# Performance work log

Hardware: AMD Instinct MI355X
Metric: run time of the kernel (lower is better)

## Reference

```python
import jax, jax.numpy as jnp
import numpy as np

EMBED = 1024
HEADS = 16
HEAD_DIM = EMBED // HEADS


def setup_inputs() -> dict:
    key = jax.random.key(0)
    ks = jax.random.split(key, 8)
    B, S = 2, 2048
    inp = {
        "values": jax.random.normal(ks[0], (B, S, EMBED), jnp.float32),
        "keys": jax.random.normal(ks[1], (B, S, EMBED), jnp.float32),
        "queries": jax.random.normal(ks[2], (B, S, EMBED), jnp.float32),
        # per-head projection weights (torch Linear: y = x @ W.T), shared across heads
        "Wv": jax.random.normal(ks[3], (HEAD_DIM, HEAD_DIM), jnp.float32) / np.sqrt(HEAD_DIM),
        "Wk": jax.random.normal(ks[4], (HEAD_DIM, HEAD_DIM), jnp.float32) / np.sqrt(HEAD_DIM),
        "Wq": jax.random.normal(ks[5], (HEAD_DIM, HEAD_DIM), jnp.float32) / np.sqrt(HEAD_DIM),
        "Wo": jax.random.normal(ks[6], (EMBED, EMBED), jnp.float32) / np.sqrt(EMBED),
        "bo": jax.random.normal(ks[7], (EMBED,), jnp.float32) * 0.02,
    }
    return inp


def reference(values, keys, queries, Wv, Wk, Wq, Wo, bo):
    B, S, _ = queries.shape
    # split heads: (B, H, S, D)
    def split(x):
        return x.reshape(B, -1, HEADS, HEAD_DIM).transpose(0, 2, 1, 3)
    v, k, q = split(values), split(keys), split(queries)
    # per-head linear projections (no bias): x @ W.T
    v = jnp.einsum('bhsd,ed->bhse', v, Wv)
    k = jnp.einsum('bhsd,ed->bhse', k, Wk)
    q = jnp.einsum('bhsd,ed->bhse', q, Wq)
    # scaled dot-product attention (naive, full matrix)
    scores = jnp.einsum('bhqd,bhkd->bhqk', q, k) / jnp.sqrt(jnp.float32(HEAD_DIM))
    attn = jax.nn.softmax(scores, axis=-1)
    out = jnp.einsum('bhqk,bhkd->bhqd', attn, v)
    # merge heads and output projection
    out = out.transpose(0, 2, 1, 3).reshape(B, S, EMBED)
    return out @ Wo.T + bo
```

## Files before the change

kernel.cpp:

```cpp
#include <hip/hip_runtime.h>
#include <stdint.h>

#define HEADS 16
#define HD    64
#define SEQ   2048
#define BATCH 2
#define EMB   1024

using short8  = __attribute__((ext_vector_type(8))) short;
using float4v = __attribute__((ext_vector_type(4))) float;

__device__ __forceinline__ unsigned int f2bfr(float f) {
    return (__float_as_uint(f) + 0x8000u) >> 16;
}

__device__ __forceinline__ unsigned int dpp_xor1(unsigned int x) {
    return (unsigned int)__builtin_amdgcn_update_dpp(0, (int)x, 0xB1, 0xF, 0xF, true);
}

__global__ __launch_bounds__(256) void cvt_wo_kernel(const float* __restrict__ Wo,
                                                     unsigned short* __restrict__ Wob) {
    int i = (blockIdx.x * 256 + threadIdx.x) * 4;
    float4 v = *(const float4*)(Wo + i);
    uint2 o;
    o.x = f2bfr(v.x) | (f2bfr(v.y) << 16);
    o.y = f2bfr(v.z) | (f2bfr(v.w) << 16);
    *(uint2*)(Wob + i) = o;
}

__global__ __launch_bounds__(256) void proj_kernel(
    const float* __restrict__ Vx, const float* __restrict__ Kx, const float* __restrict__ Qx,
    const float* __restrict__ Wv, const float* __restrict__ Wk, const float* __restrict__ Wq,
    unsigned short* __restrict__ Qp, unsigned short* __restrict__ Kp,
    unsigned short* __restrict__ Vt) {
    __shared__ __align__(16) unsigned short Ws[64 * 72];
    __shared__ __align__(16) unsigned short xs[64 * 72];
    __shared__ __align__(16) unsigned short vt2[64 * 72];

    const int t = threadIdx.x, w = t >> 6, lane = t & 63, cl = lane & 15, quad = lane >> 4;
    const int z  = blockIdx.z;
    const int bh = blockIdx.y;
    const int b  = bh >> 4, h = bh & 15;
    const int s0 = blockIdx.x * 64;

    const float* x = (z == 0) ? Qx : (z == 1) ? Kx : Vx;
    const float* W = (z == 0) ? Wq : (z == 1) ? Wk : Wv;
    const float scale = (z == 0) ? 0.18033688011112044f : 1.0f;

#pragma unroll
    for (int rep = 0; rep < 4; ++rep) {
        int idx = rep * 1024 + t * 4;
        int e = idx >> 6, d0 = idx & 63;
        float4 w4 = *(const float4*)(W + idx);
        uint2 pk;
        pk.x = f2bfr(w4.x * scale) | (f2bfr(w4.y * scale) << 16);
        pk.y = f2bfr(w4.z * scale) | (f2bfr(w4.w * scale) << 16);
        *(uint2*)(&Ws[e * 72 + d0]) = pk;

        int s = e;
        float4 v4 = *(const float4*)(x + (size_t)(b * SEQ + s0 + s) * EMB + h * 64 + d0);
        uint2 px;
        px.x = f2bfr(v4.x) | (f2bfr(v4.y) << 16);
        px.y = f2bfr(v4.z) | (f2bfr(v4.w) << 16);
        *(uint2*)(&xs[s * 72 + d0]) = px;
    }
    __syncthreads();

    short8 a0 = *(const short8*)(&xs[(w * 16 + cl) * 72 + quad * 8]);
    short8 a1 = *(const short8*)(&xs[(w * 16 + cl) * 72 + 32 + quad * 8]);
    float4v c[4];
#pragma unroll
    for (int nt = 0; nt < 4; ++nt) c[nt] = (float4v){0.f, 0.f, 0.f, 0.f};
#pragma unroll
    for (int nt = 0; nt < 4; ++nt) {
        short8 b0 = *(const short8*)(&Ws[(nt * 16 + cl) * 72 + quad * 8]);
        c[nt] = __builtin_amdgcn_mfma_f32_16x16x32_bf16(a0, b0, c[nt], 0, 0, 0);
        short8 b1 = *(const short8*)(&Ws[(nt * 16 + cl) * 72 + 32 + quad * 8]);
        c[nt] = __builtin_amdgcn_mfma_f32_16x16x32_bf16(a1, b1, c[nt], 0, 0, 0);
    }

    if (z < 2) {
#pragma unroll
        for (int nt = 0; nt < 4; ++nt)
#pragma unroll
            for (int r = 0; r < 4; ++r)
                xs[(w * 16 + quad * 4 + r) * 72 + nt * 16 + cl] =
                    (unsigned short)f2bfr(c[nt][r]);
        unsigned short* outp = (z == 0) ? Qp : Kp;
        int sl = w * 16 + (lane >> 2), c0 = (lane & 3) * 16;
        uint4 o0 = *(const uint4*)(&xs[sl * 72 + c0]);
        uint4 o1 = *(const uint4*)(&xs[sl * 72 + c0 + 8]);
        size_t base = ((size_t)bh * SEQ + s0 + sl) * 64 + c0;
        *(uint4*)(outp + base)     = o0;
        *(uint4*)(outp + base + 8) = o1;
    } else {
#pragma unroll
        for (int nt = 0; nt < 4; ++nt)
#pragma unroll
            for (int r = 0; r < 4; ++r)
                vt2[(nt * 16 + cl) * 72 + w * 16 + quad * 4 + r] =
                    (unsigned short)f2bfr(c[nt][r]);
        __syncthreads();
        int e = t >> 2, sc0 = (t & 3) * 16;
        uint4 o0 = *(const uint4*)(&vt2[e * 72 + sc0]);
        uint4 o1 = *(const uint4*)(&vt2[e * 72 + sc0 + 8]);
        size_t base = ((size_t)bh * 64 + e) * SEQ + s0 + sc0;
        *(uint4*)(Vt + base)     = o0;
        *(uint4*)(Vt + base + 8) = o1;
    }
}

__global__ __launch_bounds__(256) void attn_kernel(
    const unsigned short* __restrict__ Qp, const unsigned short* __restrict__ Kp,
    const unsigned short* __restrict__ Vt, unsigned short* __restrict__ AO) {
    __shared__ __align__(16) unsigned short Ks[2][64 * 72];
    __shared__ __align__(16) unsigned short Vs[2][64 * 72];
    __shared__ __align__(16) unsigned short Ps[4][32 * 72];

    const int t = threadIdx.x;
    const int w = t >> 6, lane = t & 63, cl = lane & 15, quad = lane >> 4;
    const int bh = blockIdx.y;
    const int q0 = blockIdx.x * 128;
    const size_t hbase = (size_t)bh * SEQ * 64;
    const unsigned short* Kbase = Kp + hbase;
    const unsigned short* Vbase = Vt + hbase;

    short8 aq[2][2];
#pragma unroll
    for (int qt = 0; qt < 2; ++qt) {
        size_t rbase = hbase + (size_t)(q0 + w * 32 + qt * 16 + cl) * 64 + quad * 8;
        aq[qt][0] = *(const short8*)(Qp + rbase);
        aq[qt][1] = *(const short8*)(Qp + rbase + 32);
    }

    short8 ones;
#pragma unroll
    for (int i = 0; i < 8; ++i) ones[i] = (short)0x3F80;

    float4v acc[2][5];
#pragma unroll
    for (int qt = 0; qt < 2; ++qt)
#pragma unroll
        for (int nt = 0; nt < 5; ++nt) acc[qt][nt] = (float4v){0.f, 0.f, 0.f, 0.f};

    const int srow = t >> 3;
    const int scol = (t & 7) * 8;

    uint4 kreg[2], vreg[2];
#pragma unroll
    for (int p = 0; p < 2; ++p) {
        int row = srow + p * 32;
        kreg[p] = *(const uint4*)(Kbase + row * 64 + scol);
        vreg[p] = *(const uint4*)(Vbase + (size_t)row * SEQ + scol);
    }

    const int even = ((lane & 1) == 0);
    const unsigned int psel = even ? 0x03020706u : 0x07060302u;
    const int evoff = even ? 0 : 16;
    unsigned int* Pw = (unsigned int*)Ps[w];

    for (int kc = 0; kc < SEQ / 64; ++kc) {
        const int buf = kc & 1;
#pragma unroll
        for (int p = 0; p < 2; ++p) {
            int row = srow + p * 32;
            *(uint4*)(&Ks[buf][row * 72 + scol]) = kreg[p];
            *(uint4*)(&Vs[buf][row * 72 + scol]) = vreg[p];
        }
        __syncthreads();
        if (kc + 1 < SEQ / 64) {
#pragma unroll
            for (int p = 0; p < 2; ++p) {
                int row = srow + p * 32;
                kreg[p] = *(const uint4*)(Kbase + (size_t)(kc + 1) * 4096 + row * 64 + scol);
                vreg[p] = *(const uint4*)(Vbase + (size_t)row * SEQ + (kc + 1) * 64 + scol);
            }
        }

        float4v c[2][4];
#pragma unroll
        for (int qt = 0; qt < 2; ++qt)
#pragma unroll
            for (int nt = 0; nt < 4; ++nt) c[qt][nt] = (float4v){0.f, 0.f, 0.f, 0.f};
#pragma unroll
        for (int nt = 0; nt < 4; ++nt) {
            short8 bk0 = *(const short8*)(&Ks[buf][(nt * 16 + cl) * 72 + quad * 8]);
            short8 bk1 = *(const short8*)(&Ks[buf][(nt * 16 + cl) * 72 + 32 + quad * 8]);
            c[0][nt] = __builtin_amdgcn_mfma_f32_16x16x32_bf16(aq[0][0], bk0, c[0][nt], 0, 0, 0);
            c[0][nt] = __builtin_amdgcn_mfma_f32_16x16x32_bf16(aq[0][1], bk1, c[0][nt], 0, 0, 0);
            c[1][nt] = __builtin_amdgcn_mfma_f32_16x16x32_bf16(aq[1][0], bk0, c[1][nt], 0, 0, 0);
            c[1][nt] = __builtin_amdgcn_mfma_f32_16x16x32_bf16(aq[1][1], bk1, c[1][nt], 0, 0, 0);
        }

#pragma unroll
        for (int qt = 0; qt < 2; ++qt) {
#pragma unroll
            for (int r = 0; r < 4; ++r) {
                unsigned int rr[4], wd[4];
#pragma unroll
                for (int nt = 0; nt < 4; ++nt)
                    rr[nt] = __float_as_uint(__builtin_amdgcn_exp2f(c[qt][nt][r])) + 0x8000u;
#pragma unroll
                for (int nt = 0; nt < 4; ++nt) {
                    unsigned int nb = dpp_xor1(rr[nt]);
                    wd[nt] = __builtin_amdgcn_perm(rr[nt], nb, psel);
                }
                unsigned int wa = even ? wd[0] : wd[2];
                unsigned int wb = even ? wd[1] : wd[3];
                int dwbase = (qt * 16 + quad * 4 + r) * 36 + evoff + (cl >> 1);
                Pw[dwbase]     = wa;
                Pw[dwbase + 8] = wb;
            }
        }

#pragma unroll
        for (int s2i = 0; s2i < 2; ++s2i) {
            short8 ap0 = *(const short8*)(&Ps[w][cl * 72 + s2i * 32 + quad * 8]);
            short8 ap1 = *(const short8*)(&Ps[w][(16 + cl) * 72 + s2i * 32 + quad * 8]);
#pragma unroll
            for (int nt = 0; nt < 4; ++nt) {
                short8 bv = *(const short8*)(&Vs[buf][(nt * 16 + cl) * 72 + s2i * 32 + quad * 8]);
                acc[0][nt] = __builtin_amdgcn_mfma_f32_16x16x32_bf16(ap0, bv, acc[0][nt], 0, 0, 0);
                acc[1][nt] = __builtin_amdgcn_mfma_f32_16x16x32_bf16(ap1, bv, acc[1][nt], 0, 0, 0);
            }
            acc[0][4] = __builtin_amdgcn_mfma_f32_16x16x32_bf16(ap0, ones, acc[0][4], 0, 0, 0);
            acc[1][4] = __builtin_amdgcn_mfma_f32_16x16x32_bf16(ap1, ones, acc[1][4], 0, 0, 0);
        }
    }

#pragma unroll
    for (int qt = 0; qt < 2; ++qt) {
        float inv[4];
#pragma unroll
        for (int r = 0; r < 4; ++r) inv[r] = 1.0f / acc[qt][4][r];
#pragma unroll
        for (int nt = 0; nt < 4; ++nt) {
#pragma unroll
            for (int r = 0; r < 4; ++r) {
                int row = q0 + w * 32 + qt * 16 + quad * 4 + r;
                AO[hbase + (size_t)row * 64 + nt * 16 + cl] =
                    (unsigned short)f2bfr(acc[qt][nt][r] * inv[r]);
            }
        }
    }
}

__global__ __launch_bounds__(256) void outproj_kernel(
    const unsigned short* __restrict__ AO, const unsigned short* __restrict__ Wob,
    const float* __restrict__ bo, float* __restrict__ out) {
    __shared__ __align__(16) unsigned short As[2][64 * 72];
    __shared__ __align__(16) unsigned short Bs[2][64 * 72];

    const int t = threadIdx.x, w = t >> 6, lane = t & 63, cl = lane & 15, quad = lane >> 4;
    const int e0 = blockIdx.x * 64;
    const int m0 = blockIdx.y * 64;
    const int srow = t >> 3, scol = (t & 7) * 8;

    float4v c[4];
#pragma unroll
    for (int nt = 0; nt < 4; ++nt) c[nt] = (float4v){0.f, 0.f, 0.f, 0.f};

    uint4 areg[2], breg[2];
#pragma unroll
    for (int p = 0; p < 2; ++p) {
        int i = srow + p * 32;
        int r = m0 + i, b = r >> 11, s = r & 2047;
        areg[p] = *(const uint4*)(AO + ((size_t)(b * 16 + 0) * SEQ + s) * 64 + scol);
        breg[p] = *(const uint4*)(Wob + (size_t)(e0 + i) * EMB + scol);
    }

    for (int hc = 0; hc < 16; ++hc) {
        const int buf = hc & 1;
#pragma unroll
        for (int p = 0; p < 2; ++p) {
            int i = srow + p * 32;
            *(uint4*)(&As[buf][i * 72 + scol]) = areg[p];
            *(uint4*)(&Bs[buf][i * 72 + scol]) = breg[p];
        }
        __syncthreads();
        if (hc + 1 < 16) {
#pragma unroll
            for (int p = 0; p < 2; ++p) {
                int i = srow + p * 32;
                int r = m0 + i, b = r >> 11, s = r & 2047;
                areg[p] = *(const uint4*)(AO + ((size_t)(b * 16 + hc + 1) * SEQ + s) * 64 + scol);
                breg[p] = *(const uint4*)(Wob + (size_t)(e0 + i) * EMB + (hc + 1) * 64 + scol);
            }
        }
#pragma unroll
        for (int s2i = 0; s2i < 2; ++s2i) {
            short8 a = *(const short8*)(&As[buf][(w * 16 + cl) * 72 + s2i * 32 + quad * 8]);
#pragma unroll
            for (int nt = 0; nt < 4; ++nt) {
                short8 bb = *(const short8*)(&Bs[buf][(nt * 16 + cl) * 72 + s2i * 32 + quad * 8]);
                c[nt] = __builtin_amdgcn_mfma_f32_16x16x32_bf16(a, bb, c[nt], 0, 0, 0);
            }
        }
    }

#pragma unroll
    for (int nt = 0; nt < 4; ++nt) {
        float bias = bo[e0 + nt * 16 + cl];
#pragma unroll
        for (int r = 0; r < 4; ++r) {
            int row = m0 + w * 16 + quad * 4 + r;
            out[(size_t)row * EMB + e0 + nt * 16 + cl] = c[nt][r] + bias;
        }
    }
}

extern "C" void kernel_launch(void* const* d_in, const int* in_sizes, int n_in,
                              void* d_out, int out_size, void* d_ws, size_t ws_size,
                              hipStream_t stream) {
    const float* values  = (const float*)d_in[0];
    const float* keys    = (const float*)d_in[1];
    const float* queries = (const float*)d_in[2];
    const float* Wv = (const float*)d_in[3];
    const float* Wk = (const float*)d_in[4];
    const float* Wq = (const float*)d_in[5];
    const float* Wo = (const float*)d_in[6];
    const float* bo = (const float*)d_in[7];
    float* out = (float*)d_out;

    char* ws = (char*)d_ws;
    unsigned short* Qp  = (unsigned short*)(ws);
    unsigned short* Kp  = (unsigned short*)(ws + (8u  << 20));
    unsigned short* Vt  = (unsigned short*)(ws + (16u << 20));
    unsigned short* AO  = (unsigned short*)(ws + (24u << 20));
    unsigned short* Wob = (unsigned short*)(ws + (32u << 20));

    cvt_wo_kernel<<<dim3(1024), dim3(256), 0, stream>>>(Wo, Wob);
    proj_kernel<<<dim3(SEQ / 64, BATCH * HEADS, 3), dim3(256), 0, stream>>>(
        values, keys, queries, Wv, Wk, Wq, Qp, Kp, Vt);
    attn_kernel<<<dim3(SEQ / 128, BATCH * HEADS), dim3(256), 0, stream>>>(Qp, Kp, Vt, AO);
    outproj_kernel<<<dim3(EMB / 64, (BATCH * SEQ) / 64), dim3(256), 0, stream>>>(
        AO, Wob, bo, out);
}
```

Baseline: 262.6 us.

## Fold Wo conversion into projection launch, single-buffer LDS, and repack P stores

Removes the separate Wo-to-bf16 kernel by adding a fourth z-slice to the projection grid, which saves one launch. The attention and output-projection kernels go from double-buffered to single-buffered LDS with an extra barrier per iteration, and attention gets a launch-bounds occupancy hint of 4 blocks. The P-tile write is repacked into 64-bit stores using fewer DPP ops, and V columns are permuted via keyslot to match the new P column order. Single buffering cuts LDS use so more blocks can be resident, but each iteration now pays an extra sync.

```diff
diff --git a/kernel.cpp b/kernel.cpp
--- a/kernel.cpp
+++ b/kernel.cpp
@@ -18,21 +18,16 @@
     return (unsigned int)__builtin_amdgcn_update_dpp(0, (int)x, 0xB1, 0xF, 0xF, true);
 }
 
-__global__ __launch_bounds__(256) void cvt_wo_kernel(const float* __restrict__ Wo,
-                                                     unsigned short* __restrict__ Wob) {
-    int i = (blockIdx.x * 256 + threadIdx.x) * 4;
-    float4 v = *(const float4*)(Wo + i);
-    uint2 o;
-    o.x = f2bfr(v.x) | (f2bfr(v.y) << 16);
-    o.y = f2bfr(v.z) | (f2bfr(v.w) << 16);
-    *(uint2*)(Wob + i) = o;
+__device__ __forceinline__ int keyslot(int k) {
+    return ((k & 14) << 2) | ((k >> 4) << 1) | (k & 1);
 }
 
 __global__ __launch_bounds__(256) void proj_kernel(
     const float* __restrict__ Vx, const float* __restrict__ Kx, const float* __restrict__ Qx,
     const float* __restrict__ Wv, const float* __restrict__ Wk, const float* __restrict__ Wq,
+    const float* __restrict__ Wo,
     unsigned short* __restrict__ Qp, unsigned short* __restrict__ Kp,
-    unsigned short* __restrict__ Vt) {
+    unsigned short* __restrict__ Vt, unsigned short* __restrict__ Wob) {
     __shared__ __align__(16) unsigned short Ws[64 * 72];
     __shared__ __align__(16) unsigned short xs[64 * 72];
     __shared__ __align__(16) unsigned short vt2[64 * 72];
@@ -42,6 +37,16 @@
     const int bh = blockIdx.y;
     const int b  = bh >> 4, h = bh & 15;
     const int s0 = blockIdx.x * 64;
+
+    if (z == 3) {
+        int idx = (bh * 32 + blockIdx.x) * 1024 + t * 4;
+        float4 v = *(const float4*)(Wo + idx);
+        uint2 o;
+        o.x = f2bfr(v.x) | (f2bfr(v.y) << 16);
+        o.y = f2bfr(v.z) | (f2bfr(v.w) << 16);
+        *(uint2*)(Wob + idx) = o;
+        return;
+    }
 
     const float* x = (z == 0) ? Qx : (z == 1) ? Kx : Vx;
     const float* W = (z == 0) ? Wq : (z == 1) ? Wk : Wv;
@@ -97,9 +102,10 @@
 #pragma unroll
         for (int nt = 0; nt < 4; ++nt)
 #pragma unroll
-            for (int r = 0; r < 4; ++r)
-                vt2[(nt * 16 + cl) * 72 + w * 16 + quad * 4 + r] =
-                    (unsigned short)f2bfr(c[nt][r]);
+            for (int r = 0; r < 4; ++r) {
+                int s = w * 16 + quad * 4 + r;
+                vt2[(nt * 16 + cl) * 72 + keyslot(s)] = (unsigned short)f2bfr(c[nt][r]);
+            }
         __syncthreads();
         int e = t >> 2, sc0 = (t & 3) * 16;
         uint4 o0 = *(const uint4*)(&vt2[e * 72 + sc0]);
@@ -110,11 +116,11 @@
     }
 }
 
-__global__ __launch_bounds__(256) void attn_kernel(
+__global__ __launch_bounds__(256, 4) void attn_kernel(
     const unsigned short* __restrict__ Qp, const unsigned short* __restrict__ Kp,
     const unsigned short* __restrict__ Vt, unsigned short* __restrict__ AO) {
-    __shared__ __align__(16) unsigned short Ks[2][64 * 72];
-    __shared__ __align__(16) unsigned short Vs[2][64 * 72];
+    __shared__ __align__(16) unsigned short Ks[64 * 72];
+    __shared__ __align__(16) unsigned short Vs[64 * 72];
     __shared__ __align__(16) unsigned short Ps[4][32 * 72];
 
     const int t = threadIdx.x;
@@ -156,17 +162,14 @@
 
     const int even = ((lane & 1) == 0);
     const unsigned int psel = even ? 0x03020706u : 0x07060302u;
-    const int evoff = even ? 0 : 16;
-    unsigned int* Pw = (unsigned int*)Ps[w];
+    const int p2 = (cl >> 1) * 2 + (even ? 0 : 1);
+    uint2* Pw2 = (uint2*)Ps[w];
 
     for (int kc = 0; kc < SEQ / 64; ++kc) {
-        const int buf = kc & 1;
-#pragma unroll
-        for (int p = 0; p < 2; ++p) {
-            int row = srow + p * 32;
-            *(uint4*)(&Ks[buf][row * 72 + scol]) = kreg[p];
-            *(uint4*)(&Vs[buf][row * 72 + scol]) = vreg[p];
-        }
+        *(uint4*)(&Ks[srow * 72 + scol])        = kreg[0];
+        *(uint4*)(&Ks[(srow + 32) * 72 + scol]) = kreg[1];
+        *(uint4*)(&Vs[srow * 72 + scol])        = vreg[0];
+        *(uint4*)(&Vs[(srow + 32) * 72 + scol]) = vreg[1];
         __syncthreads();
         if (kc + 1 < SEQ / 64) {
 #pragma unroll
@@ -184,8 +187,8 @@
             for (int nt = 0; nt < 4; ++nt) c[qt][nt] = (float4v){0.f, 0.f, 0.f, 0.f};
 #pragma unroll
         for (int nt = 0; nt < 4; ++nt) {
-            short8 bk0 = *(const short8*)(&Ks[buf][(nt * 16 + cl) * 72 + quad * 8]);
-            short8 bk1 = *(const short8*)(&Ks[buf][(nt * 16 + cl) * 72 + 32 + quad * 8]);
+            short8 bk0 = *(const short8*)(&Ks[(nt * 16 + cl) * 72 + quad * 8]);
+            short8 bk1 = *(const short8*)(&Ks[(nt * 16 + cl) * 72 + 32 + quad * 8]);
             c[0][nt] = __builtin_amdgcn_mfma_f32_16x16x32_bf16(aq[0][0], bk0, c[0][nt], 0, 0, 0);
             c[0][nt] = __builtin_amdgcn_mfma_f32_16x16x32_bf16(aq[0][1], bk1, c[0][nt], 0, 0, 0);
             c[1][nt] = __builtin_amdgcn_mfma_f32_16x16x32_bf16(aq[1][0], bk0, c[1][nt], 0, 0, 0);
@@ -196,20 +199,19 @@
         for (int qt = 0; qt < 2; ++qt) {
 #pragma unroll
             for (int r = 0; r < 4; ++r) {
-                unsigned int rr[4], wd[4];
+                unsigned int rr[4];
 #pragma unroll
                 for (int nt = 0; nt < 4; ++nt)
                     rr[nt] = __float_as_uint(__builtin_amdgcn_exp2f(c[qt][nt][r])) + 0x8000u;
-#pragma unroll
-                for (int nt = 0; nt < 4; ++nt) {
-                    unsigned int nb = dpp_xor1(rr[nt]);
-                    wd[nt] = __builtin_amdgcn_perm(rr[nt], nb, psel);
-                }
-                unsigned int wa = even ? wd[0] : wd[2];
-                unsigned int wb = even ? wd[1] : wd[3];
-                int dwbase = (qt * 16 + quad * 4 + r) * 36 + evoff + (cl >> 1);
-                Pw[dwbase]     = wa;
-                Pw[dwbase + 8] = wb;
+                unsigned int g1 = dpp_xor1(even ? rr[2] : rr[0]);
+                unsigned int g2 = dpp_xor1(even ? rr[3] : rr[1]);
+                unsigned int s0 = even ? rr[0] : rr[2];
+                unsigned int s1 = even ? rr[1] : rr[3];
+                uint2 wd;
+                wd.x = __builtin_amdgcn_perm(s0, g1, psel);
+                wd.y = __builtin_amdgcn_perm(s1, g2, psel);
+                int row = qt * 16 + quad * 4 + r;
+                Pw2[row * 18 + p2] = wd;
             }
         }
 
@@ -219,13 +221,14 @@
             short8 ap1 = *(const short8*)(&Ps[w][(16 + cl) * 72 + s2i * 32 + quad * 8]);
 #pragma unroll
             for (int nt = 0; nt < 4; ++nt) {
-                short8 bv = *(const short8*)(&Vs[buf][(nt * 16 + cl) * 72 + s2i * 32 + quad * 8]);
+                short8 bv = *(const short8*)(&Vs[(nt * 16 + cl) * 72 + s2i * 32 + quad * 8]);
                 acc[0][nt] = __builtin_amdgcn_mfma_f32_16x16x32_bf16(ap0, bv, acc[0][nt], 0, 0, 0);
                 acc[1][nt] = __builtin_amdgcn_mfma_f32_16x16x32_bf16(ap1, bv, acc[1][nt], 0, 0, 0);
             }
             acc[0][4] = __builtin_amdgcn_mfma_f32_16x16x32_bf16(ap0, ones, acc[0][4], 0, 0, 0);
             acc[1][4] = __builtin_amdgcn_mfma_f32_16x16x32_bf16(ap1, ones, acc[1][4], 0, 0, 0);
         }
+        __syncthreads();
     }
 
 #pragma unroll
@@ -248,8 +251,8 @@
 __global__ __launch_bounds__(256) void outproj_kernel(
     const unsigned short* __restrict__ AO, const unsigned short* __restrict__ Wob,
     const float* __restrict__ bo, float* __restrict__ out) {
-    __shared__ __align__(16) unsigned short As[2][64 * 72];
-    __shared__ __align__(16) unsigned short Bs[2][64 * 72];
+    __shared__ __align__(16) unsigned short As[64 * 72];
+    __shared__ __align__(16) unsigned short Bs[64 * 72];
 
     const int t = threadIdx.x, w = t >> 6, lane = t & 63, cl = lane & 15, quad = lane >> 4;
     const int e0 = blockIdx.x * 64;
@@ -270,12 +273,11 @@
     }
 
     for (int hc = 0; hc < 16; ++hc) {
-        const int buf = hc & 1;
 #pragma unroll
         for (int p = 0; p < 2; ++p) {
             int i = srow + p * 32;
-            *(uint4*)(&As[buf][i * 72 + scol]) = areg[p];
-            *(uint4*)(&Bs[buf][i * 72 + scol]) = breg[p];
+            *(uint4*)(&As[i * 72 + scol]) = areg[p];
+            *(uint4*)(&Bs[i * 72 + scol]) = breg[p];
         }
         __syncthreads();
         if (hc + 1 < 16) {
@@ -289,13 +291,14 @@
         }
 #pragma unroll
         for (int s2i = 0; s2i < 2; ++s2i) {
-            short8 a = *(const short8*)(&As[buf][(w * 16 + cl) * 72 + s2i * 32 + quad * 8]);
+            short8 a = *(const short8*)(&As[(w * 16 + cl) * 72 + s2i * 32 + quad * 8]);
 #pragma unroll
             for (int nt = 0; nt < 4; ++nt) {
-                short8 bb = *(const short8*)(&Bs[buf][(nt * 16 + cl) * 72 + s2i * 32 + quad * 8]);
+                short8 bb = *(const short8*)(&Bs[(nt * 16 + cl) * 72 + s2i * 32 + quad * 8]);
                 c[nt] = __builtin_amdgcn_mfma_f32_16x16x32_bf16(a, bb, c[nt], 0, 0, 0);
             }
         }
+        __syncthreads();
     }
 
 #pragma unroll
@@ -329,9 +332,8 @@
     unsigned short* AO  = (unsigned short*)(ws + (24u << 20));
     unsigned short* Wob = (unsigned short*)(ws + (32u << 20));
 
-    cvt_wo_kernel<<<dim3(1024), dim3(256), 0, stream>>>(Wo, Wob);
-    proj_kernel<<<dim3(SEQ / 64, BATCH * HEADS, 3), dim3(256), 0, stream>>>(
-        values, keys, queries, Wv, Wk, Wq, Qp, Kp, Vt);
+    proj_kernel<<<dim3(SEQ / 64, BATCH * HEADS, 4), dim3(256), 0, stream>>>(
+        values, keys, queries, Wv, Wk, Wq, Wo, Qp, Kp, Vt, Wob);
     attn_kernel<<<dim3(SEQ / 128, BATCH * HEADS), dim3(256), 0, stream>>>(Qp, Kp, Vt, AO);
     outproj_kernel<<<dim3(EMB / 64, (BATCH * SEQ) / 64), dim3(256), 0, stream>>>(
         AO, Wob, bo, out);
```

Result: slower. 293.0 us (+11.6%).
